# Kernel tuning notes

Measured on AMD Instinct MI355X. Metric: run time of the kernel, lower is better.

## Reference

```python
import jax, jax.numpy as jnp
import numpy as np

B, S, D, H = 4, 2048, 1024, 16
HD = D // H  # 64

def setup_inputs() -> dict:
    key = jax.random.key(0)
    ks = jax.random.split(key, 8)
    scale = 0.02
    return {
        "hidden_states": jax.random.normal(ks[0], (B, S, D), dtype=jnp.float32),
        "attention_mask": jnp.zeros((B, 1, 1, S), dtype=jnp.float32),
        "Wq": jax.random.normal(ks[1], (D, D), dtype=jnp.float32) * scale,
        "bq": jnp.zeros((D,), dtype=jnp.float32),
        "Wk": jax.random.normal(ks[2], (D, D), dtype=jnp.float32) * scale,
        "bk": jnp.zeros((D,), dtype=jnp.float32),
        "Wv": jax.random.normal(ks[3], (D, D), dtype=jnp.float32) * scale,
        "bv": jnp.zeros((D,), dtype=jnp.float32),
    }

def _split_heads(x):
    # [B,S,D] -> [B,H,S,HD]
    return x.reshape(B, S, H, HD).transpose(0, 2, 1, 3)

def reference(hidden_states, attention_mask, Wq, bq, Wk, bk, Wv, bv):
    q = _split_heads(hidden_states @ Wq.T + bq)
    k = _split_heads(hidden_states @ Wk.T + bk)
    v = _split_heads(hidden_states @ Wv.T + bv)
    scores = jnp.einsum('bhqd,bhkd->bhqk', q, k) / jnp.sqrt(jnp.float32(HD))
    scores = scores + attention_mask  # additive mask, broadcast [B,1,1,S]
    probs = jax.nn.softmax(scores, axis=-1)
    ctx = jnp.einsum('bhqk,bhkd->bhqd', probs, v)
    ctx = ctx.transpose(0, 2, 1, 3).reshape(B, S, D)
    return ctx
```

## Files before the change

### kernel.cpp

```cpp
#include <hip/hip_runtime.h>
#include <hip/hip_bf16.h>

typedef __bf16 bf16;
typedef __bf16 bf16x8 __attribute__((ext_vector_type(8)));
typedef __bf16 bf16x4 __attribute__((ext_vector_type(4)));
typedef float f32x4 __attribute__((ext_vector_type(4)));
typedef unsigned int u32;
typedef unsigned short u16;

constexpr int B_ = 4, S = 2048, D = 1024, H = 16, HD = 64;
constexpr int M = B_ * S;

#define MFMA(a, b, c) __builtin_amdgcn_mfma_f32_16x16x32_bf16(a, b, c, 0, 0, 0)

__device__ inline void gl_lds16(const bf16* g, bf16* l) {
  __builtin_amdgcn_global_load_lds(
      (const __attribute__((address_space(1))) u32*)g,
      (__attribute__((address_space(3))) u32*)l, 16, 0, 0);
}

__device__ inline bf16x8 load8(const void* base, size_t idx, bool isf32) {
  if (isf32) {
    const float* p = (const float*)base + idx;
    const float4 a = *(const float4*)p;
    const float4 b = *(const float4*)(p + 4);
    bf16x8 r;
    r[0] = (bf16)a.x; r[1] = (bf16)a.y; r[2] = (bf16)a.z; r[3] = (bf16)a.w;
    r[4] = (bf16)b.x; r[5] = (bf16)b.y; r[6] = (bf16)b.z; r[7] = (bf16)b.w;
    return r;
  }
  return *(const bf16x8*)((const bf16*)base + idx);
}
__device__ inline float load1(const void* base, size_t idx, bool isf32) {
  return isf32 ? ((const float*)base)[idx] : (float)((const bf16*)base)[idx];
}
__device__ inline f32x4 load4(const void* base, size_t idx, bool isf32) {
  if (isf32) {
    const float4 v = *(const float4*)((const float*)base + idx);
    return {v.x, v.y, v.z, v.w};
  }
  const bf16x4 v = *(const bf16x4*)((const bf16*)base + idx);
  return {(float)v[0], (float)v[1], (float)v[2], (float)v[3]};
}

__global__ __launch_bounds__(256) void detect_dtype(const uint4* __restrict__ X,
                                                    int* __restrict__ flag) {
  bool hit = false;
  for (int i = blockIdx.x * 256 + threadIdx.x; i < 32768; i += 64 * 256) {
    const uint4 v = X[i];
    const u32 w[4] = {v.x, v.y, v.z, v.w};
#pragma unroll
    for (int j = 0; j < 4; j++) {
      if (((w[j] >> 7) & 0xFFu) == 0xFFu) hit = true;
      if (((w[j] >> 23) & 0xFFu) == 0xFFu) hit = true;
    }
  }
  __shared__ int s;
  if (threadIdx.x == 0) s = 0;
  __syncthreads();
  if (hit) atomicOr(&s, 1);
  __syncthreads();
  if (threadIdx.x == 0 && s) atomicOr(flag, 1);
}

__global__ __launch_bounds__(256) void detect_mask(const uint4* __restrict__ Mk,
                                                   int* __restrict__ flag) {
  const bool isf32 = (*flag & 1) != 0;
  const int n4 = (B_ * S * (isf32 ? 4 : 2)) / 16;
  bool nz = false;
  for (int i = blockIdx.x * 256 + threadIdx.x; i < n4; i += 8 * 256) {
    const uint4 v = Mk[i];
    nz |= ((v.x | v.y | v.z | v.w) != 0u);
  }
  __shared__ int s;
  if (threadIdx.x == 0) s = 0;
  __syncthreads();
  if (nz) atomicOr(&s, 1);
  __syncthreads();
  if (threadIdx.x == 0 && s) atomicOr(flag, 2);
}

__global__ __launch_bounds__(256) void convert_inputs(
    const void* __restrict__ X, const void* __restrict__ W0,
    const void* __restrict__ W1, const void* __restrict__ W2,
    bf16* __restrict__ Xb, bf16* __restrict__ Wb,
    const int* __restrict__ flagp) {
  if ((*flagp & 1) == 0) return;
  const int seg = blockIdx.y;
  const size_t n = (seg == 0) ? (size_t)M * D : (size_t)D * D;
  const size_t i0 = ((size_t)blockIdx.x * 256 + threadIdx.x) * 8;
  if (i0 >= n) return;
  const void* src = seg == 0 ? X : seg == 1 ? W0 : seg == 2 ? W1 : W2;
  bf16* dst = seg == 0 ? Xb : Wb + (size_t)(seg - 1) * D * D;
  *(bf16x8*)(dst + i0) = load8(src, i0, true);
}

__global__ __launch_bounds__(256) void qkv_gemm(
    const void* __restrict__ X0, const bf16* __restrict__ Xb,
    const void* __restrict__ W0, const void* __restrict__ W1, const void* __restrict__ W2,
    const void* __restrict__ b0, const void* __restrict__ b1, const void* __restrict__ b2,
    bf16* __restrict__ Qo, bf16* __restrict__ Ko, bf16* __restrict__ Vo,
    const bf16* __restrict__ Wb, const int* __restrict__ flagp) {
  const int z = blockIdx.z;
  const bool isf32 = (*flagp & 1) != 0;
  const void* Worig = z == 0 ? W0 : z == 1 ? W1 : W2;
  const void* bias  = z == 0 ? b0 : z == 1 ? b1 : b2;
  bf16* out         = z == 0 ? Qo : z == 1 ? Ko : Vo;
  const bf16* Xs = isf32 ? Xb : (const bf16*)X0;
  const bf16* Ws = isf32 ? (Wb + (size_t)z * D * D) : (const bf16*)Worig;

  __shared__ __align__(16) bf16 As[128 * 32];
  __shared__ __align__(16) bf16 Bs[128 * 32];
  const int tid = threadIdx.x, lane = tid & 63, wave = tid >> 6;
  const int q16 = lane & 15, quad = lane >> 4;
  const int wm = (wave & 1) * 64, wn = (wave >> 1) * 64;
  const int bm = blockIdx.x * 128, bn = blockIdx.y * 128;
  const int r0 = tid >> 2, kg = (tid & 3) * 8;

  f32x4 acc[4][4] = {};

  for (int k0 = 0; k0 < D; k0 += 32) {
    __syncthreads();
    gl_lds16(Xs + (size_t)(bm + r0) * D + k0 + kg,      As + wave * 512 + lane * 8);
    gl_lds16(Xs + (size_t)(bm + 64 + r0) * D + k0 + kg, As + (4 + wave) * 512 + lane * 8);
    gl_lds16(Ws + (size_t)(bn + r0) * D + k0 + kg,      Bs + wave * 512 + lane * 8);
    gl_lds16(Ws + (size_t)(bn + 64 + r0) * D + k0 + kg, Bs + (4 + wave) * 512 + lane * 8);
    __syncthreads();
    bf16x8 af[4], bfr[4];
#pragma unroll
    for (int i = 0; i < 4; i++) {
      af[i]  = *(const bf16x8*)(As + (wm + i * 16 + q16) * 32 + quad * 8);
      bfr[i] = *(const bf16x8*)(Bs + (wn + i * 16 + q16) * 32 + quad * 8);
    }
#pragma unroll
    for (int mi = 0; mi < 4; mi++)
#pragma unroll
      for (int ni = 0; ni < 4; ni++)
        acc[mi][ni] = MFMA(af[mi], bfr[ni], acc[mi][ni]);
  }

  const float scl = (z == 0) ? 0.125f * 1.44269504f : 1.0f;
#pragma unroll
  for (int mi = 0; mi < 4; mi++) {
#pragma unroll
    for (int ni = 0; ni < 4; ni++) {
      const int gn = bn + wn + ni * 16 + q16;
      const float bb = load1(bias, gn, isf32);
      const int h = gn >> 6, hd = gn & 63;
      const int gm0 = bm + wm + mi * 16 + quad * 4;
      const int bidx = gm0 >> 11, s0 = gm0 & 2047;
      if (z == 2) {
        bf16x4 v4;
#pragma unroll
        for (int r = 0; r < 4; r++) v4[r] = (bf16)(acc[mi][ni][r] + bb);
        *(bf16x4*)(out + ((size_t)(bidx * H + h) * HD + hd) * S + s0) = v4;
      } else {
#pragma unroll
        for (int r = 0; r < 4; r++)
          out[((size_t)(bidx * H + h) * S + (s0 + r)) * HD + hd] = (bf16)((acc[mi][ni][r] + bb) * scl);
      }
    }
  }
}

__global__ __launch_bounds__(256, 2) void attn(
    const bf16* __restrict__ Q, const bf16* __restrict__ K,
    const bf16* __restrict__ Vt, const void* __restrict__ mask,
    void* __restrict__ outv, const int* __restrict__ flagp) {
  const int fl = *flagp;
  const bool isf32 = (fl & 1) != 0;
  const bool havemask = (fl & 2) != 0;
  const int tid = threadIdx.x, lane = tid & 63, wave = tid >> 6;
  const int q16 = lane & 15, quad = lane >> 4;

  const int bid = blockIdx.x;
  const int xcd = bid & 7, l = bid >> 3;
  const int bh = (xcd << 3) | (l & 7);
  const int qchunk = l >> 3;
  const int b = bh >> 4, h = bh & 15;
  const int qbase = qchunk * 256 + wave * 64;
  const float L2E = 1.44269504f;

  bf16x8 qf[4][2];
#pragma unroll
  for (int qs = 0; qs < 4; qs++) {
    const bf16* qr = Q + ((size_t)bh * S + qbase + qs * 16 + q16) * HD;
    qf[qs][0] = *(const bf16x8*)(qr + quad * 8);
    qf[qs][1] = *(const bf16x8*)(qr + 32 + quad * 8);
  }

  f32x4 o[4][4] = {};
  float racc[4] = {};

  const bf16* Kb = K + (size_t)bh * S * HD;
  const bf16* Vb = Vt + (size_t)bh * HD * S;
  const int kprow = 8 * (q16 >> 2) + (q16 & 3);
  const size_t mbase = (size_t)b * S;

  for (int t = 0; t < 32; t++) {
    const int kt = t * 64;
    bf16x8 kf[4][2];
#pragma unroll
    for (int ki = 0; ki < 4; ki++) {
      const bf16* kr = Kb + (size_t)(kt + 32 * (ki >> 1) + 4 * (ki & 1) + kprow) * HD;
      kf[ki][0] = *(const bf16x8*)(kr + quad * 8);
      kf[ki][1] = *(const bf16x8*)(kr + 32 + quad * 8);
    }
    bf16x8 vf[4][2];
#pragma unroll
    for (int hi = 0; hi < 4; hi++) {
      const bf16* vr = Vb + (size_t)(hi * 16 + q16) * S + kt;
      vf[hi][0] = *(const bf16x8*)(vr + quad * 8);
      vf[hi][1] = *(const bf16x8*)(vr + 32 + quad * 8);
    }
    f32x4 mk[4];
    if (havemask) {
#pragma unroll
      for (int ki = 0; ki < 4; ki++) {
        f32x4 mv = load4(mask, mbase + kt + 32 * (ki >> 1) + 4 * (ki & 1) + 8 * quad, isf32);
#pragma unroll
        for (int r = 0; r < 4; r++) mk[ki][r] = mv[r] * L2E;
      }
    }

#pragma unroll
    for (int qs = 0; qs < 4; qs++) {
      f32x4 sc[4];
      __builtin_amdgcn_s_setprio(1);
#pragma unroll
      for (int ki = 0; ki < 4; ki++) {
        f32x4 zz = {0.f, 0.f, 0.f, 0.f};
        zz = MFMA(kf[ki][0], qf[qs][0], zz);
        sc[ki] = MFMA(kf[ki][1], qf[qs][1], zz);
      }
      __builtin_amdgcn_s_setprio(0);
      bf16x8 pb[2];
      float rs = 0.f;
#pragma unroll
      for (int ki = 0; ki < 4; ki++) {
        const int hh = ki >> 1, half = (ki & 1) * 4;
        float p0, p1, p2, p3;
        if (havemask) {
          p0 = __builtin_amdgcn_exp2f(sc[ki][0] + mk[ki][0]);
          p1 = __builtin_amdgcn_exp2f(sc[ki][1] + mk[ki][1]);
          p2 = __builtin_amdgcn_exp2f(sc[ki][2] + mk[ki][2]);
          p3 = __builtin_amdgcn_exp2f(sc[ki][3] + mk[ki][3]);
        } else {
          p0 = __builtin_amdgcn_exp2f(sc[ki][0]);
          p1 = __builtin_amdgcn_exp2f(sc[ki][1]);
          p2 = __builtin_amdgcn_exp2f(sc[ki][2]);
          p3 = __builtin_amdgcn_exp2f(sc[ki][3]);
        }
        rs += ((p0 + p1) + (p2 + p3));
        pb[hh][half + 0] = (bf16)p0; pb[hh][half + 1] = (bf16)p1;
        pb[hh][half + 2] = (bf16)p2; pb[hh][half + 3] = (bf16)p3;
      }
      racc[qs] += rs;
      __builtin_amdgcn_s_setprio(1);
#pragma unroll
      for (int hi = 0; hi < 4; hi++) {
        o[qs][hi] = MFMA(vf[hi][0], pb[0], o[qs][hi]);
        o[qs][hi] = MFMA(vf[hi][1], pb[1], o[qs][hi]);
      }
      __builtin_amdgcn_s_setprio(0);
    }
  }

#pragma unroll
  for (int qs = 0; qs < 4; qs++) {
    racc[qs] += __shfl_xor(racc[qs], 16);
    racc[qs] += __shfl_xor(racc[qs], 32);
  }

#pragma unroll
  for (int qs = 0; qs < 4; qs++) {
    const float inv = 1.0f / racc[qs];
    const size_t row = (size_t)b * S + qbase + qs * 16 + q16;
#pragma unroll
    for (int hi = 0; hi < 4; hi++) {
      const size_t off = row * D + h * HD + hi * 16 + quad * 4;
      if (isf32) {
        float4 st;
        st.x = o[qs][hi][0] * inv; st.y = o[qs][hi][1] * inv;
        st.z = o[qs][hi][2] * inv; st.w = o[qs][hi][3] * inv;
        *(float4*)((float*)outv + off) = st;
      } else {
        bf16x4 st;
#pragma unroll
        for (int r = 0; r < 4; r++) st[r] = (bf16)(o[qs][hi][r] * inv);
        *(bf16x4*)((bf16*)outv + off) = st;
      }
    }
  }
}

extern "C" void kernel_launch(void* const* d_in, const int* in_sizes, int n_in,
                              void* d_out, int out_size, void* d_ws, size_t ws_size,
                              hipStream_t stream) {
  const void* X    = d_in[0];
  const void* mask = d_in[1];
  const void* Wq = d_in[2]; const void* bq = d_in[3];
  const void* Wk = d_in[4]; const void* bk = d_in[5];
  const void* Wv = d_in[6]; const void* bv = d_in[7];

  const size_t elems = (size_t)M * D;
  bf16* Qw = (bf16*)d_ws;
  bf16* Kw = Qw + elems;
  bf16* Vw = Kw + elems;
  int* flag = (int*)(Vw + elems);

  bf16* Xb = (bf16*)d_out;
  bf16* Wb = Xb + elems;

  hipMemsetAsync(flag, 0, sizeof(int), stream);
  detect_dtype<<<64, 256, 0, stream>>>((const uint4*)X, flag);
  detect_mask<<<8, 256, 0, stream>>>((const uint4*)mask, flag);
  convert_inputs<<<dim3(4096, 4), 256, 0, stream>>>(X, Wq, Wk, Wv, Xb, Wb, flag);
  qkv_gemm<<<dim3(M / 128, D / 128, 3), 256, 0, stream>>>(
      X, Xb, Wq, Wk, Wv, bq, bk, bv, Qw, Kw, Vw, Wb, flag);
  attn<<<dim3(512), 256, 0, stream>>>(Qw, Kw, Vw, mask, d_out, flag);
}
```

Baseline: 286.1 us.

## Rewrite QKV GEMM with 256x256 tiles, double-buffered swizzled LDS and ping-pong scheduling

The QKV projection GEMM moves from 128x128 tiles with 4 waves and a single-buffered K=32 LDS stage to 256x256 tiles with 8 waves. It uses K=64 double-buffered LDS stages loaded directly from global memory, and an XOR swizzle to avoid LDS bank conflicts. MFMA bursts are interleaved with barriers and setprio, so loads for tile k+2 overlap compute on tile k. The goal is higher arithmetic intensity and overlap of memory with compute. In exchange it uses 128KB of LDS and more registers, and the grid shrinks to 384 blocks, which may leave some CUs idle.

```diff
diff --git a/kernel.cpp b/kernel.cpp
--- a/kernel.cpp
+++ b/kernel.cpp
@@ -41,6 +41,10 @@
   }
   const bf16x4 v = *(const bf16x4*)((const bf16*)base + idx);
   return {(float)v[0], (float)v[1], (float)v[2], (float)v[3]};
+}
+
+__device__ inline bf16x8 swzfrag(const bf16* buf, int row, int cb) {
+  return *(const bf16x8*)((const char*)buf + row * 128 + (cb ^ ((row & 7) << 4)));
 }
 
 __global__ __launch_bounds__(256) void detect_dtype(const uint4* __restrict__ X,
@@ -95,7 +99,7 @@
   *(bf16x8*)(dst + i0) = load8(src, i0, true);
 }
 
-__global__ __launch_bounds__(256) void qkv_gemm(
+__global__ __launch_bounds__(512, 2) void qkv_gemm(
     const void* __restrict__ X0, const bf16* __restrict__ Xb,
     const void* __restrict__ W0, const void* __restrict__ W1, const void* __restrict__ W2,
     const void* __restrict__ b0, const void* __restrict__ b1, const void* __restrict__ b2,
@@ -109,55 +113,123 @@
   const bf16* Xs = isf32 ? Xb : (const bf16*)X0;
   const bf16* Ws = isf32 ? (Wb + (size_t)z * D * D) : (const bf16*)Worig;
 
-  __shared__ __align__(16) bf16 As[128 * 32];
-  __shared__ __align__(16) bf16 Bs[128 * 32];
-  const int tid = threadIdx.x, lane = tid & 63, wave = tid >> 6;
+  __shared__ __align__(16) bf16 Asm[2][16384];
+  __shared__ __align__(16) bf16 Bsm[2][16384];
+
+  const int tid = threadIdx.x, lane = tid & 63;
   const int q16 = lane & 15, quad = lane >> 4;
-  const int wm = (wave & 1) * 64, wn = (wave >> 1) * 64;
-  const int bm = blockIdx.x * 128, bn = blockIdx.y * 128;
-  const int r0 = tid >> 2, kg = (tid & 3) * 8;
-
-  f32x4 acc[4][4] = {};
-
-  for (int k0 = 0; k0 < D; k0 += 32) {
-    __syncthreads();
-    gl_lds16(Xs + (size_t)(bm + r0) * D + k0 + kg,      As + wave * 512 + lane * 8);
-    gl_lds16(Xs + (size_t)(bm + 64 + r0) * D + k0 + kg, As + (4 + wave) * 512 + lane * 8);
-    gl_lds16(Ws + (size_t)(bn + r0) * D + k0 + kg,      Bs + wave * 512 + lane * 8);
-    gl_lds16(Ws + (size_t)(bn + 64 + r0) * D + k0 + kg, Bs + (4 + wave) * 512 + lane * 8);
-    __syncthreads();
-    bf16x8 af[4], bfr[4];
-#pragma unroll
-    for (int i = 0; i < 4; i++) {
-      af[i]  = *(const bf16x8*)(As + (wm + i * 16 + q16) * 32 + quad * 8);
-      bfr[i] = *(const bf16x8*)(Bs + (wn + i * 16 + q16) * 32 + quad * 8);
-    }
-#pragma unroll
-    for (int mi = 0; mi < 4; mi++)
-#pragma unroll
-      for (int ni = 0; ni < 4; ni++)
-        acc[mi][ni] = MFMA(af[mi], bfr[ni], acc[mi][ni]);
-  }
+  const int wid = tid >> 6, wr = wid >> 2, wc = wid & 3;
+  const int bm = blockIdx.x * 256, bn = blockIdx.y * 256;
+
+  const int srow = tid >> 3;
+  const int cel = ((((tid & 7) * 16) ^ ((srow & 7) << 4)) >> 1);
+  int aOff[4], bOff[4];
+#pragma unroll
+  for (int j = 0; j < 4; j++) {
+    aOff[j] = (bm + j * 64 + srow) * D + cel;
+    bOff[j] = (bn + j * 64 + srow) * D + cel;
+  }
+
+  f32x4 acc[8][4] = {};
+
+#define STAGE(sel, ktile)                                                     \
+  {                                                                           \
+    const int ko = (ktile) * 64;                                              \
+    _Pragma("unroll") for (int j = 0; j < 4; j++)                             \
+        gl_lds16(Xs + (size_t)(aOff[j] + ko), &Asm[sel][j * 4096 + tid * 8]); \
+    _Pragma("unroll") for (int j = 0; j < 4; j++)                             \
+        gl_lds16(Ws + (size_t)(bOff[j] + ko), &Bsm[sel][j * 4096 + tid * 8]); \
+  }
+
+  STAGE(0, 0);
+  STAGE(1, 1);
+  asm volatile("s_waitcnt vmcnt(8)" ::: "memory");
+  __builtin_amdgcn_s_barrier();
+
+  const int NT = D / 64;
+  for (int kt = 0; kt < NT; ++kt) {
+    const bf16* Ab = Asm[kt & 1];
+    const bf16* Bb = Bsm[kt & 1];
+    bf16x8 a[8], u, v;
+#pragma unroll
+    for (int mf = 0; mf < 8; mf++) a[mf] = swzfrag(Ab, wr * 128 + mf * 16 + q16, quad * 16);
+    u = swzfrag(Bb, wc * 64 + q16, quad * 16);
+    v = swzfrag(Bb, wc * 64 + 16 + q16, quad * 16);
+    __builtin_amdgcn_s_barrier();
+    __builtin_amdgcn_s_setprio(1);
+#pragma unroll
+    for (int mf = 0; mf < 8; mf++) {
+      acc[mf][0] = MFMA(a[mf], u, acc[mf][0]);
+      acc[mf][1] = MFMA(a[mf], v, acc[mf][1]);
+    }
+    __builtin_amdgcn_s_setprio(0);
+    __builtin_amdgcn_s_barrier();
+    u = swzfrag(Bb, wc * 64 + 32 + q16, quad * 16);
+    v = swzfrag(Bb, wc * 64 + 48 + q16, quad * 16);
+    __builtin_amdgcn_s_barrier();
+    __builtin_amdgcn_s_setprio(1);
+#pragma unroll
+    for (int mf = 0; mf < 8; mf++) {
+      acc[mf][2] = MFMA(a[mf], u, acc[mf][2]);
+      acc[mf][3] = MFMA(a[mf], v, acc[mf][3]);
+    }
+    __builtin_amdgcn_s_setprio(0);
+    __builtin_amdgcn_s_barrier();
+#pragma unroll
+    for (int mf = 0; mf < 8; mf++) a[mf] = swzfrag(Ab, wr * 128 + mf * 16 + q16, 64 + quad * 16);
+    u = swzfrag(Bb, wc * 64 + q16, 64 + quad * 16);
+    v = swzfrag(Bb, wc * 64 + 16 + q16, 64 + quad * 16);
+    __builtin_amdgcn_s_barrier();
+    __builtin_amdgcn_s_setprio(1);
+#pragma unroll
+    for (int mf = 0; mf < 8; mf++) {
+      acc[mf][0] = MFMA(a[mf], u, acc[mf][0]);
+      acc[mf][1] = MFMA(a[mf], v, acc[mf][1]);
+    }
+    __builtin_amdgcn_s_setprio(0);
+    __builtin_amdgcn_s_barrier();
+    u = swzfrag(Bb, wc * 64 + 32 + q16, 64 + quad * 16);
+    v = swzfrag(Bb, wc * 64 + 48 + q16, 64 + quad * 16);
+    __builtin_amdgcn_s_barrier();
+    __builtin_amdgcn_s_setprio(1);
+#pragma unroll
+    for (int mf = 0; mf < 8; mf++) {
+      acc[mf][2] = MFMA(a[mf], u, acc[mf][2]);
+      acc[mf][3] = MFMA(a[mf], v, acc[mf][3]);
+    }
+    __builtin_amdgcn_s_setprio(0);
+    asm volatile("s_waitcnt lgkmcnt(0)" ::: "memory");
+    __builtin_amdgcn_s_barrier();
+    if (kt + 2 < NT) {
+      STAGE(kt & 1, kt + 2);
+      asm volatile("s_waitcnt vmcnt(8)" ::: "memory");
+    } else if (kt + 1 < NT) {
+      asm volatile("s_waitcnt vmcnt(0)" ::: "memory");
+    }
+    __builtin_amdgcn_s_barrier();
+  }
+#undef STAGE
 
   const float scl = (z == 0) ? 0.125f * 1.44269504f : 1.0f;
 #pragma unroll
-  for (int mi = 0; mi < 4; mi++) {
-#pragma unroll
-    for (int ni = 0; ni < 4; ni++) {
-      const int gn = bn + wn + ni * 16 + q16;
+  for (int mf = 0; mf < 8; mf++) {
+#pragma unroll
+    for (int nf = 0; nf < 4; nf++) {
+      const int gn = bn + wc * 64 + nf * 16 + q16;
       const float bb = load1(bias, gn, isf32);
       const int h = gn >> 6, hd = gn & 63;
-      const int gm0 = bm + wm + mi * 16 + quad * 4;
+      const int gm0 = bm + wr * 128 + mf * 16 + quad * 4;
       const int bidx = gm0 >> 11, s0 = gm0 & 2047;
       if (z == 2) {
         bf16x4 v4;
 #pragma unroll
-        for (int r = 0; r < 4; r++) v4[r] = (bf16)(acc[mi][ni][r] + bb);
+        for (int r = 0; r < 4; r++) v4[r] = (bf16)(acc[mf][nf][r] + bb);
         *(bf16x4*)(out + ((size_t)(bidx * H + h) * HD + hd) * S + s0) = v4;
       } else {
 #pragma unroll
         for (int r = 0; r < 4; r++)
-          out[((size_t)(bidx * H + h) * S + (s0 + r)) * HD + hd] = (bf16)((acc[mi][ni][r] + bb) * scl);
+          out[((size_t)(bidx * H + h) * S + (s0 + r)) * HD + hd] =
+              (bf16)((acc[mf][nf][r] + bb) * scl);
       }
     }
   }
@@ -316,7 +388,7 @@
   detect_dtype<<<64, 256, 0, stream>>>((const uint4*)X, flag);
   detect_mask<<<8, 256, 0, stream>>>((const uint4*)mask, flag);
   convert_inputs<<<dim3(4096, 4), 256, 0, stream>>>(X, Wq, Wk, Wv, Xb, Wb, flag);
-  qkv_gemm<<<dim3(M / 128, D / 128, 3), 256, 0, stream>>>(
+  qkv_gemm<<<dim3(M / 256, D / 256, 3), 512, 0, stream>>>(
       X, Xb, Wq, Wk, Wv, bq, bk, bv, Qw, Kw, Vw, Wb, flag);
   attn<<<dim3(512), 256, 0, stream>>>(Qw, Kw, Vw, mask, d_out, flag);
 }
```

New measurement: 311.8 us. 1.09x slower.
